# Performance work log

Measured on AMD Instinct MI355X. Metric: run time of the kernel, lower is better.

The kernel has to match this reference:

```python
import jax, jax.numpy as jnp
import numpy as np
import math

B, L, CS, CZ = 1, 512, 256, 128
H, CH, PQ, PV = 8, 32, 4, 8
NUM_BLOCKS = 8
CAT = H * CH + H * PV * 3 + H * PV + H * CZ  # 1536


def _ln(x, g, b, eps=1e-5):
    mu = jnp.mean(x, -1, keepdims=True)
    var = jnp.mean((x - mu) ** 2, -1, keepdims=True)
    return (x - mu) * jax.lax.rsqrt(var + eps) * g + b


def _quat_to_rot(bq, cq, dq):
    # BackboneUpdate: quaternion with implicit a=1, normalized (AF2 Alg. 23)
    norm = jnp.sqrt(1.0 + bq * bq + cq * cq + dq * dq)
    a = 1.0 / norm
    b = bq / norm
    c = cq / norm
    d = dq / norm
    return jnp.stack([
        jnp.stack([a * a + b * b - c * c - d * d, 2 * (b * c - a * d), 2 * (b * d + a * c)], -1),
        jnp.stack([2 * (b * c + a * d), a * a - b * b + c * c - d * d, 2 * (c * d - a * b)], -1),
        jnp.stack([2 * (b * d - a * c), 2 * (c * d + a * b), a * a - b * b - c * c + d * d], -1),
    ], -2)


def _forward(s, z, mask, ln_s_g, ln_s_b, ln_z_g, ln_z_b, w_init, b_init,
             ln_ipa_g, ln_ipa_b, ln_tr_g, ln_tr_b,
             wq, bq, wk, bk, wv, bv, wqp, bqp, wkp, bkp, wvp, bvp,
             wpb, head_w, wo, bo, wt1, bt1, wt2, bt2, wt3, bt3, wbb, bbb):
    s0 = _ln(s, ln_s_g, ln_s_b)
    zn = _ln(z, ln_z_g, ln_z_b)
    sc = s0 @ w_init + b_init
    R = jnp.broadcast_to(jnp.eye(3, dtype=s.dtype), (B, L, 3, 3))
    t = jnp.zeros((B, L, 3), s.dtype)
    wL = math.sqrt(1.0 / 3.0)
    wC = math.sqrt(2.0 / (9.0 * PQ))
    gamma = jax.nn.softplus(head_w)  # [H]
    pair_bias = jnp.einsum('bijc,ch->bhij', zn, wpb)
    mask_bias = (mask[:, None, None, :] - 1.0) * 1e9
    for i in range(NUM_BLOCKS):
        # ---- Invariant Point Attention (AF2 Alg. 22, shared weights) ----
        q = (sc @ wq + bq).reshape(B, L, H, CH)
        k = (sc @ wk + bk).reshape(B, L, H, CH)
        v = (sc @ wv + bv).reshape(B, L, H, CH)
        qp = (sc @ wqp + bqp).reshape(B, L, H, PQ, 3)
        kp = (sc @ wkp + bkp).reshape(B, L, H, PQ, 3)
        vp = (sc @ wvp + bvp).reshape(B, L, H, PV, 3)
        tb = t[:, :, None, None, :]
        qpg = jnp.einsum('blij,blhpj->blhpi', R, qp) + tb  # local -> global
        kpg = jnp.einsum('blij,blhpj->blhpi', R, kp) + tb
        vpg = jnp.einsum('blij,blhpj->blhpi', R, vp) + tb
        scal = jnp.einsum('bihc,bjhc->bhij', q, k) / math.sqrt(CH)
        # sum_p ||qpg_i - kpg_j||^2 via |q|^2 + |k|^2 - 2 q.k (avoids [B,L,L,H,P,3])
        qk = jnp.einsum('bihpx,bjhpx->bhij', qpg, kpg)
        qn = jnp.moveaxis(jnp.sum(qpg ** 2, axis=(-2, -1)), -1, 1)  # [B,H,L]
        kn = jnp.moveaxis(jnp.sum(kpg ** 2, axis=(-2, -1)), -1, 1)
        d2 = qn[..., :, None] + kn[..., None, :] - 2.0 * qk  # [B,H,L,L]
        logits = wL * (scal + pair_bias - 0.5 * wC * gamma[None, :, None, None] * d2) + mask_bias
        a = jax.nn.softmax(logits, axis=-1)
        o = jnp.einsum('bhij,bjhc->bihc', a, v).reshape(B, L, H * CH)
        optg = jnp.einsum('bhij,bjhpx->bihpx', a, vpg)
        optl = jnp.einsum('blji,blhpj->blhpi', R, optg - tb)  # R^T (o - t)
        onrm = jnp.sqrt(jnp.sum(optl ** 2, -1) + 1e-8)  # [B,L,H,PV]
        opair = jnp.einsum('bhij,bijc->bihc', a, zn).reshape(B, L, H * CZ)
        cat = jnp.concatenate([o, optl.reshape(B, L, H * PV * 3), onrm.reshape(B, L, H * PV), opair], -1)
        ipa_up = cat @ wo + bo
        sc = _ln(sc + ipa_up, ln_ipa_g, ln_ipa_b)  # dropout = identity (eval)
        # ---- transition ----
        tr = jax.nn.relu(sc @ wt1 + bt1)
        tr = jax.nn.relu(tr @ wt2 + bt2)
        tr = (tr @ wt3 + bt3) * mask[..., None]
        sc = _ln(sc + tr, ln_tr_g, ln_tr_b)
        # ---- backbone update + frame composition ----
        upd = sc @ wbb + bbb  # [B,L,6]
        dR = _quat_to_rot(upd[..., 0], upd[..., 1], upd[..., 2])
        dt = upd[..., 3:6] * mask[..., None]
        t = jnp.einsum('blij,blj->bli', R, dt) + t
        R = jnp.einsum('blij,bljk->blik', R, dR)
        if i < NUM_BLOCKS - 1:
            R = jax.lax.stop_gradient(R)  # stop_rotation_gradients
    return sc, R, t


def setup_inputs() -> dict:
    key = jax.random.key(0)
    ks = jax.random.split(key, 20)
    w = lambda k, shape, sc=0.05: jax.random.normal(k, shape, jnp.float32) * sc
    inp = dict(
        s=jax.random.normal(ks[0], (B, L, CS), jnp.float32),
        z=jax.random.normal(ks[1], (B, L, L, CZ), jnp.float32),
        mask=jnp.ones((B, L), jnp.float32),
        ln_s_g=jnp.ones((CS,), jnp.float32), ln_s_b=jnp.zeros((CS,), jnp.float32),
        ln_z_g=jnp.ones((CZ,), jnp.float32), ln_z_b=jnp.zeros((CZ,), jnp.float32),
        w_init=w(ks[2], (CS, CS)), b_init=jnp.zeros((CS,), jnp.float32),
        ln_ipa_g=jnp.ones((CS,), jnp.float32), ln_ipa_b=jnp.zeros((CS,), jnp.float32),
        ln_tr_g=jnp.ones((CS,), jnp.float32), ln_tr_b=jnp.zeros((CS,), jnp.float32),
        wq=w(ks[3], (CS, H * CH)), bq=jnp.zeros((H * CH,), jnp.float32),
        wk=w(ks[4], (CS, H * CH)), bk=jnp.zeros((H * CH,), jnp.float32),
        wv=w(ks[5], (CS, H * CH)), bv=jnp.zeros((H * CH,), jnp.float32),
        wqp=w(ks[6], (CS, H * PQ * 3)), bqp=jnp.zeros((H * PQ * 3,), jnp.float32),
        wkp=w(ks[7], (CS, H * PQ * 3)), bkp=jnp.zeros((H * PQ * 3,), jnp.float32),
        wvp=w(ks[8], (CS, H * PV * 3)), bvp=jnp.zeros((H * PV * 3,), jnp.float32),
        wpb=w(ks[9], (CZ, H)),
        head_w=jnp.zeros((H,), jnp.float32),
        wo=w(ks[10], (CAT, CS), 0.02), bo=jnp.zeros((CS,), jnp.float32),
        wt1=w(ks[11], (CS, CS)), bt1=jnp.zeros((CS,), jnp.float32),
        wt2=w(ks[12], (CS, CS)), bt2=jnp.zeros((CS,), jnp.float32),
        wt3=w(ks[13], (CS, CS)), bt3=jnp.zeros((CS,), jnp.float32),
        wbb=w(ks[14], (CS, 6)), bbb=jnp.zeros((6,), jnp.float32),
    )
    return inp


def reference(s, z, mask, ln_s_g, ln_s_b, ln_z_g, ln_z_b, w_init, b_init,
              ln_ipa_g, ln_ipa_b, ln_tr_g, ln_tr_b,
              wq, bq, wk, bk, wv, bv, wqp, bqp, wkp, bkp, wvp, bvp,
              wpb, head_w, wo, bo, wt1, bt1, wt2, bt2, wt3, bt3, wbb, bbb):
    return _forward(s, z, mask, ln_s_g, ln_s_b, ln_z_g, ln_z_b, w_init, b_init,
                    ln_ipa_g, ln_ipa_b, ln_tr_g, ln_tr_b,
                    wq, bq, wk, bk, wv, bv, wqp, bqp, wkp, bkp, wvp, bvp,
                    wpb, head_w, wo, bo, wt1, bt1, wt2, bt2, wt3, bt3, wbb, bbb)
```

## Files before the change

### kernel.cpp

```cpp
#include <hip/hip_runtime.h>
#include <hip/hip_bf16.h>
#include <hip/hip_fp16.h>
#include <math.h>

#define Lq 512
#define CSd 256
#define CZd 128
#define Hd 8
#define CHd 32
#define PQd 4
#define PVd 8
#define CATd 1536
#define NPROJ 1152

typedef __attribute__((ext_vector_type(4))) float floatx4;
typedef __attribute__((ext_vector_type(8))) short shortx8;

#define OFF_SC      0
#define OFF_PB      393216
#define OFF_P       1441792
#define OFF_QN      2031616
#define OFF_KN      2035712
#define OFF_A16     2039808
#define OFF_CAT     4136960
#define OFF_S0      4923392
#define OFF_R       5054464
#define OFF_T       5059072
#define OFF_GAMMA   5060608
#define OFF_MASKB   5060616
#define OFF_BCAT    5061128
#define OFF_WINITP  5062280
#define OFF_WT1P    5127816
#define OFF_WT2P    5193352
#define OFF_WT3P    5258888
#define OFF_WOP     5324424
#define OFF_WCATP   5717640
#define OFF_QP      6012552
#define OFF_KP      6274696
#define OFF_VP      6536840
#define OFF_ZNT     6798984

#define WLC 0.57735026918962576f
#define WCC 0.23570226039551584f
#define ISC 0.17677669529663687f

__device__ __forceinline__ float wave_sum(float v){
  #pragma unroll
  for (int m=32; m; m>>=1) v += __shfl_xor(v, m);
  return v;
}
__device__ __forceinline__ short f2bf(float v){
  __hip_bfloat16 h = (__hip_bfloat16)v;
  return __builtin_bit_cast(short, h);
}
__device__ __forceinline__ float bf2f(short s){
  unsigned u = ((unsigned)(unsigned short)s) << 16;
  return __builtin_bit_cast(float, u);
}
__device__ __forceinline__ __hip_bfloat16 s2b(short s){
  return __builtin_bit_cast(__hip_bfloat16, s);
}

__global__ __launch_bounds__(256) void k_setup(
    const float* __restrict__ bq, const float* __restrict__ bk, const float* __restrict__ bv,
    const float* __restrict__ bqp, const float* __restrict__ bkp, const float* __restrict__ bvp,
    const float* __restrict__ head_w, const float* __restrict__ mask,
    float* __restrict__ bcat, float* __restrict__ gamma,
    float* __restrict__ maskb, float* __restrict__ R, float* __restrict__ t){
  int k = blockIdx.x*256 + threadIdx.x;
  if (k < NPROJ){
    float v;
    if      (k < 256) v = bq[k];
    else if (k < 512) v = bk[k-256];
    else if (k < 768) v = bv[k-512];
    else if (k < 864) v = bqp[k-768];
    else if (k < 960) v = bkp[k-864];
    else              v = bvp[k-960];
    bcat[k] = v;
    return;
  }
  k -= NPROJ;
  if (k < Hd){ gamma[k] = log1pf(expf(head_w[k])); return; }
  k -= Hd;
  if (k < Lq){ maskb[k] = (mask[k] - 1.f)*1e9f; return; }
  k -= Lq;
  if (k < Lq){
    #pragma unroll
    for (int ii=0; ii<9; ii++) R[k*9+ii] = (ii==0||ii==4||ii==8) ? 1.f : 0.f;
    t[k*3] = 0.f; t[k*3+1] = 0.f; t[k*3+2] = 0.f;
  }
}

__global__ __launch_bounds__(256) void k_pack(
    const float* __restrict__ W, int K, int N, __hip_bfloat16* __restrict__ out){
  int idx = blockIdx.x*256 + threadIdx.x;
  if (idx >= K*N) return;
  int j = idx & 7, lane = (idx>>3) & 63, rest = idx >> 9;
  int nt = N >> 4;
  int tn = rest % nt, tk = rest / nt;
  int k = tk*32 + (lane>>4)*8 + j;
  int n = tn*16 + (lane&15);
  float v = W[(size_t)k*N + n];
  short h = f2bf(v);
  short l = f2bf(v - bf2f(h));
  size_t base = (size_t)rest*1024 + (idx & 511);
  out[base]       = s2b(h);
  out[base + 512] = s2b(l);
}

__global__ __launch_bounds__(256) void k_pack_cat(
    const float* __restrict__ wq, const float* __restrict__ wk, const float* __restrict__ wv,
    const float* __restrict__ wqp, const float* __restrict__ wkp, const float* __restrict__ wvp,
    __hip_bfloat16* __restrict__ out){
  int idx = blockIdx.x*256 + threadIdx.x;
  if (idx >= CSd*NPROJ) return;
  int j = idx & 7, lane = (idx>>3) & 63, rest = idx >> 9;
  const int nt = NPROJ >> 4;
  int tn = rest % nt, tk = rest / nt;
  int k = tk*32 + (lane>>4)*8 + j;
  int n = tn*16 + (lane&15);
  float v;
  if      (n < 256) v = wq[k*256 + n];
  else if (n < 512) v = wk[k*256 + n-256];
  else if (n < 768) v = wv[k*256 + n-512];
  else if (n < 864) v = wqp[k*96 + n-768];
  else if (n < 960) v = wkp[k*96 + n-864];
  else              v = wvp[k*192 + n-960];
  short h = f2bf(v);
  short l = f2bf(v - bf2f(h));
  size_t base = (size_t)rest*1024 + (idx & 511);
  out[base]       = s2b(h);
  out[base + 512] = s2b(l);
}

template<int NST>
__global__ __launch_bounds__(256) void k_gemm_mfma(
    const float* __restrict__ A, int K,
    const __hip_bfloat16* __restrict__ Bp, int N,
    const float* __restrict__ bias,
    float* __restrict__ Cf,
    int relu, const float* __restrict__ rowscale){
  int tid = threadIdx.x;
  int wave = tid>>6, lane = tid&63;
  int i0 = blockIdx.y*64 + wave*16;
  int n0 = blockIdx.x*(NST*16);
  int quad = lane>>4, l16 = lane&15;
  floatx4 acc[NST] = {};
  const int ntiles = N >> 4;
  const float* arow = A + (size_t)(i0 + l16)*K + quad*8;
  const __hip_bfloat16* bbase = Bp + ((size_t)(n0>>4))*1024 + (size_t)(lane&63)*8;
  for (int k0=0; k0<K; k0+=32){
    float4 v0 = *(const float4*)(arow + k0);
    float4 v1 = *(const float4*)(arow + k0 + 4);
    float av[8] = {v0.x,v0.y,v0.z,v0.w,v1.x,v1.y,v1.z,v1.w};
    shortx8 ahi, alo;
    #pragma unroll
    for (int j=0; j<8; j++){
      short h = f2bf(av[j]);
      ahi[j] = h;
      alo[j] = f2bf(av[j] - bf2f(h));
    }
    const __hip_bfloat16* bt = bbase + (size_t)(k0>>5)*ntiles*1024;
    #pragma unroll
    for (int s=0; s<NST; s++){
      shortx8 bhi = *(const shortx8*)(bt + s*1024);
      shortx8 blo = *(const shortx8*)(bt + s*1024 + 512);
      acc[s] = __builtin_amdgcn_mfma_f32_16x16x32_bf16(ahi, bhi, acc[s], 0, 0, 0);
      acc[s] = __builtin_amdgcn_mfma_f32_16x16x32_bf16(alo, bhi, acc[s], 0, 0, 0);
      acc[s] = __builtin_amdgcn_mfma_f32_16x16x32_bf16(ahi, blo, acc[s], 0, 0, 0);
    }
  }
  #pragma unroll
  for (int s=0; s<NST; s++){
    int n = n0 + s*16 + l16;
    float bs = bias ? bias[n] : 0.f;
    #pragma unroll
    for (int r=0; r<4; r++){
      int m = i0 + quad*4 + r;
      float v = acc[s][r] + bs;
      if (relu) v = fmaxf(v, 0.f);
      if (rowscale) v *= rowscale[m];
      Cf[(size_t)m*N + n] = v;
    }
  }
}

__global__ __launch_bounds__(256) void k_addln(
    const float* __restrict__ x, const float* __restrict__ y,
    const float* __restrict__ g, const float* __restrict__ b,
    float* __restrict__ out){
  __shared__ float red[4];
  int row = blockIdx.x, tid = threadIdx.x;
  float v = x[row*CSd + tid];
  if (y) v += y[row*CSd + tid];
  int wid = tid>>6, lane = tid&63;
  float s = wave_sum(v);
  if (lane==0) red[wid] = s;
  __syncthreads();
  float mu = (red[0]+red[1]+red[2]+red[3]) * (1.f/CSd);
  __syncthreads();
  float d = v - mu;
  float s2 = wave_sum(d*d);
  if (lane==0) red[wid] = s2;
  __syncthreads();
  float var = (red[0]+red[1]+red[2]+red[3]) * (1.f/CSd);
  float rs = rsqrtf(var + 1e-5f);
  out[row*CSd + tid] = d*rs*g[tid] + b[tid];
}

__global__ __launch_bounds__(1024, 4) void k_lnz_pb(
    const float* __restrict__ z, const float* __restrict__ g, const float* __restrict__ b,
    const float* __restrict__ wpb, __half* __restrict__ pb, __hip_bfloat16* __restrict__ znt){
  __shared__ float Zt[64*129];
  __shared__ float wpbht[8*132];
  __shared__ float gl[128], bl[128];
  __shared__ float muL[64], rsL[64];
  int tid = threadIdx.x;
  size_t row0 = (size_t)blockIdx.x*64;
  int ib = (int)(row0 >> 9), j0 = (int)(row0 & 511);
  {
    int c = tid>>3, h = tid&7;
    wpbht[h*132 + c] = wpb[tid];
  }
  if (tid < 128){ gl[tid] = g[tid]; bl[tid] = b[tid]; }
  {
    int w = tid>>6, lane = tid&63;
    #pragma unroll
    for (int it=0; it<4; it++){
      int row = it*16 + w;
      const float2 v = *(const float2*)(z + (row0+row)*(size_t)CZd + lane*2);
      Zt[row*129 + lane*2]     = v.x;
      Zt[row*129 + lane*2 + 1] = v.y;
    }
  }
  __syncthreads();
  {
    int r = tid>>4, q = tid&15;
    int rot = 2*(q>>2);
    float S1=0.f, S2=0.f;
    float zv[8];
    #pragma unroll
    for (int i=0; i<8; i++){
      int ii = (i + rot) & 7;
      float v = Zt[r*129 + q*8 + ii];
      zv[i] = v;
      S1 += v; S2 += v*v;
    }
    S1 += __shfl_xor(S1,1); S2 += __shfl_xor(S2,1);
    S1 += __shfl_xor(S1,2); S2 += __shfl_xor(S2,2);
    S1 += __shfl_xor(S1,4); S2 += __shfl_xor(S2,4);
    S1 += __shfl_xor(S1,8); S2 += __shfl_xor(S2,8);
    float mu = S1 * (1.f/128.f);
    float var = S2 * (1.f/128.f) - mu*mu;
    float rs = rsqrtf(var + 1e-5f);
    if (q == 0){ muL[r] = mu; rsL[r] = rs; }
    float d[8] = {};
    #pragma unroll
    for (int i=0; i<8; i++){
      int ii = (i + rot) & 7;
      int c = q*8 + ii;
      float znv = (zv[i]-mu)*rs*gl[c] + bl[c];
      #pragma unroll
      for (int h=0; h<8; h++) d[h] += znv * wpbht[h*132 + c];
    }
    #pragma unroll
    for (int h=0; h<8; h++){
      d[h] += __shfl_xor(d[h],1);
      d[h] += __shfl_xor(d[h],2);
      d[h] += __shfl_xor(d[h],4);
      d[h] += __shfl_xor(d[h],8);
    }
    if (q == 0){
      #pragma unroll
      for (int h=0; h<8; h++)
        pb[((size_t)(h*Lq + ib))*Lq + j0 + r] = __float2half(d[h]);
    }
  }
  __syncthreads();
  {
    int jj = (tid&31)*2, cidx = tid>>5;
    float mu0 = muL[jj],   rs0 = rsL[jj];
    float mu1 = muL[jj+1], rs1 = rsL[jj+1];
    unsigned short* zo = (unsigned short*)znt;
    #pragma unroll
    for (int it=0; it<4; it++){
      int c = it*32 + cidx;
      float gv = gl[c], bv = bl[c];
      float z0 = (Zt[jj*129 + c]     - mu0)*rs0*gv + bv;
      float z1 = (Zt[(jj+1)*129 + c] - mu1)*rs1*gv + bv;
      unsigned int o = ((unsigned int)(unsigned short)f2bf(z0)) |
                       (((unsigned int)(unsigned short)f2bf(z1)) << 16);
      *(unsigned int*)(zo + ((size_t)(ib*128 + c))*512 + j0 + jj) = o;
    }
  }
}

__global__ __launch_bounds__(256) void k_packqkv(
    const float* __restrict__ P, const float* __restrict__ R, const float* __restrict__ t,
    const float* __restrict__ gamma, int zfill,
    float* __restrict__ Qp, __hip_bfloat16* __restrict__ Kp, __hip_bfloat16* __restrict__ Vp,
    float* __restrict__ qn, float* __restrict__ kn){
  int idx = blockIdx.x*256 + threadIdx.x;
  int region = idx >> 15;
  int rem = idx & 32767;
  if (region == 0){
    int oct = rem & 7, h = (rem>>3)&7, j = rem>>6;
    float v[8] = {0.f,0.f,0.f,0.f,0.f,0.f,0.f,0.f};
    const float* Prow = P + (size_t)j*NPROJ;
    if (oct < 4){
      float4 a = *(const float4*)(Prow + 256 + h*CHd + oct*8);
      float4 b4 = *(const float4*)(Prow + 256 + h*CHd + oct*8 + 4);
      v[0]=a.x; v[1]=a.y; v[2]=a.z; v[3]=a.w; v[4]=b4.x; v[5]=b4.y; v[6]=b4.z; v[7]=b4.w;
    } else if (oct < 6){
      const float* kp = Prow + 864 + h*12;
      float4 k0 = *(const float4*)kp;
      float4 k1 = *(const float4*)(kp+4);
      float4 k2 = *(const float4*)(kp+8);
      float kv[12] = {k0.x,k0.y,k0.z,k0.w,k1.x,k1.y,k1.z,k1.w,k2.x,k2.y,k2.z,k2.w};
      float Rl[9];
      #pragma unroll
      for (int ii=0; ii<9; ii++) Rl[ii] = R[j*9+ii];
      float tv[3] = {t[j*3], t[j*3+1], t[j*3+2]};
      float gvals[12];
      #pragma unroll
      for (int p=0; p<4; p++)
        #pragma unroll
        for (int ax=0; ax<3; ax++)
          gvals[p*3+ax] = Rl[ax*3]*kv[p*3] + Rl[ax*3+1]*kv[p*3+1] + Rl[ax*3+2]*kv[p*3+2] + tv[ax];
      if (oct == 4){
        #pragma unroll
        for (int m=0; m<8; m++) v[m] = gvals[m];
      } else {
        #pragma unroll
        for (int m=0; m<4; m++) v[m] = gvals[8+m];
        float acc = 0.f;
        #pragma unroll
        for (int m=0; m<12; m++) acc += gvals[m]*gvals[m];
        kn[j*Hd + h] = acc;
      }
    } else {
      if (!zfill) return;
    }
    shortx8 hi, lo;
    #pragma unroll
    for (int m=0; m<8; m++){
      short hh = f2bf(v[m]);
      hi[m] = hh; lo[m] = f2bf(v[m] - bf2f(hh));
    }
    int kc = oct>>2, jt = j>>4, l16 = j&15, quad = oct&3;
    size_t base = (size_t)((h*2+kc)*32 + jt)*1024 + (quad*16+l16)*8;
    short* kp16 = (short*)Kp;
    *(shortx8*)(kp16 + base)       = hi;
    *(shortx8*)(kp16 + base + 512) = lo;
  } else if (region == 1){
    int n = rem & 63, h = (rem>>6)&7, jg = rem>>9;
    int jb = jg*8;
    float v[8] = {0.f,0.f,0.f,0.f,0.f,0.f,0.f,0.f};
    if (n < 32){
      #pragma unroll
      for (int m=0; m<8; m++) v[m] = P[(size_t)(jb+m)*NPROJ + 512 + h*CHd + n];
    } else if (n < 56){
      int p = (n-32)/3, ax = (n-32)%3;
      #pragma unroll
      for (int m=0; m<8; m++){
        int j = jb+m;
        const float* vp = P + (size_t)j*NPROJ + 960 + h*24 + p*3;
        const float* Rr = R + j*9 + ax*3;
        v[m] = Rr[0]*vp[0] + Rr[1]*vp[1] + Rr[2]*vp[2] + t[j*3+ax];
      }
    } else {
      if (!zfill) return;
    }
    shortx8 hi, lo;
    #pragma unroll
    for (int m=0; m<8; m++){
      short hh = f2bf(v[m]);
      hi[m] = hh; lo[m] = f2bf(v[m] - bf2f(hh));
    }
    int kc2 = jg>>2, w = n>>4, l16 = n&15, quad = jg&3;
    size_t base = (size_t)((h*16+kc2)*4 + w)*1024 + (quad*16+l16)*8;
    short* vp16 = (short*)Vp;
    *(shortx8*)(vp16 + base)       = hi;
    *(shortx8*)(vp16 + base + 512) = lo;
  } else {
    int oct = rem & 7, h = (rem>>3)&7, i = rem>>6;
    float v[8] = {0.f,0.f,0.f,0.f,0.f,0.f,0.f,0.f};
    const float* Prow = P + (size_t)i*NPROJ;
    if (oct < 4){
      float4 a = *(const float4*)(Prow + h*CHd + oct*8);
      float4 b4 = *(const float4*)(Prow + h*CHd + oct*8 + 4);
      const float sc = WLC*ISC;
      v[0]=a.x*sc; v[1]=a.y*sc; v[2]=a.z*sc; v[3]=a.w*sc;
      v[4]=b4.x*sc; v[5]=b4.y*sc; v[6]=b4.z*sc; v[7]=b4.w*sc;
    } else if (oct < 6){
      const float* qp = Prow + 768 + h*12;
      float4 k0 = *(const float4*)qp;
      float4 k1 = *(const float4*)(qp+4);
      float4 k2 = *(const float4*)(qp+8);
      float kv[12] = {k0.x,k0.y,k0.z,k0.w,k1.x,k1.y,k1.z,k1.w,k2.x,k2.y,k2.z,k2.w};
      float Rl[9];
      #pragma unroll
      for (int ii=0; ii<9; ii++) Rl[ii] = R[i*9+ii];
      float tv[3] = {t[i*3], t[i*3+1], t[i*3+2]};
      float gvals[12];
      #pragma unroll
      for (int p=0; p<4; p++)
        #pragma unroll
        for (int ax=0; ax<3; ax++)
          gvals[p*3+ax] = Rl[ax*3]*kv[p*3] + Rl[ax*3+1]*kv[p*3+1] + Rl[ax*3+2]*kv[p*3+2] + tv[ax];
      float sc = WLC*WCC*gamma[h];
      if (oct == 4){
        #pragma unroll
        for (int m=0; m<8; m++) v[m] = gvals[m]*sc;
      } else {
        #pragma unroll
        for (int m=0; m<4; m++) v[m] = gvals[8+m]*sc;
        float acc = 0.f;
        #pragma unroll
        for (int m=0; m<12; m++) acc += gvals[m]*gvals[m];
        qn[i*Hd + h] = acc;
      }
    } else {
      if (!zfill) return;
    }
    float* qrow = Qp + ((size_t)h*512 + i)*64 + oct*8;
    *(float4*)qrow       = make_float4(v[0],v[1],v[2],v[3]);
    *(float4*)(qrow + 4) = make_float4(v[4],v[5],v[6],v[7]);
  }
}

__global__ __launch_bounds__(512) void k_attn(
    const float* __restrict__ Qp, const __hip_bfloat16* __restrict__ Kp,
    const __hip_bfloat16* __restrict__ Vp,
    const float* __restrict__ qn, const float* __restrict__ kn,
    const __half* __restrict__ pb, const float* __restrict__ maskb,
    const float* __restrict__ gamma,
    const float* __restrict__ R, const float* __restrict__ t,
    __hip_bfloat16* __restrict__ a16hi,
    float* __restrict__ cat){
  __shared__ float At[16][516];
  __shared__ short AbfH[16*4*16*8];
  __shared__ short AbfL[16*4*16*8];
  __shared__ float Ot[16][36];
  __shared__ float Pv[16][68];
  __shared__ float red1[16][32];
  __shared__ float red2[16][32];
  __shared__ float invL[16];
  __shared__ float qnL[16];
  int tid = threadIdx.x;
  int i0 = blockIdx.x*16, h = blockIdx.y;
  int wave = tid>>6, lane = tid&63, quad = lane>>4, l16 = lane&15;
  int half = wave>>2, w4 = wave&3;
  float gam = gamma[h];
  float coef = 0.5f*WLC*WCC*gam;
  if (tid < 16) qnL[tid] = qn[(i0+tid)*Hd + h];
  __syncthreads();
  const float* qrow = Qp + ((size_t)h*512 + i0 + l16)*64 + quad*8;
  shortx8 qhi[2], qlo[2];
  #pragma unroll
  for (int kc=0; kc<2; kc++){
    float4 v0 = *(const float4*)(qrow + kc*32);
    float4 v1 = *(const float4*)(qrow + kc*32 + 4);
    float av[8] = {v0.x,v0.y,v0.z,v0.w,v1.x,v1.y,v1.z,v1.w};
    #pragma unroll
    for (int j=0; j<8; j++){
      short hh = f2bf(av[j]);
      qhi[kc][j] = hh; qlo[kc][j] = f2bf(av[j] - bf2f(hh));
    }
  }
  #pragma unroll
  for (int it=0; it<4; it++){
    int jt = it*8 + wave;
    floatx4 acc = {};
    #pragma unroll
    for (int kc=0; kc<2; kc++){
      const __hip_bfloat16* bt = Kp + (size_t)((h*2+kc)*32 + jt)*1024 + lane*8;
      shortx8 bhi = *(const shortx8*)bt;
      shortx8 blo = *(const shortx8*)(bt + 512);
      acc = __builtin_amdgcn_mfma_f32_16x16x32_bf16(qhi[kc], bhi, acc, 0, 0, 0);
      acc = __builtin_amdgcn_mfma_f32_16x16x32_bf16(qlo[kc], bhi, acc, 0, 0, 0);
      acc = __builtin_amdgcn_mfma_f32_16x16x32_bf16(qhi[kc], blo, acc, 0, 0, 0);
    }
    int j = jt*16 + l16;
    float knj = kn[j*Hd + h];
    float mbj = maskb[j];
    #pragma unroll
    for (int r=0; r<4; r++){
      int i = quad*4 + r;
      float pbv = __half2float(pb[((size_t)(h*Lq) + i0 + i)*Lq + j]);
      At[i][j] = acc[r] + WLC*pbv + mbj - coef*(qnL[i] + knj);
    }
  }
  __syncthreads();
  int srow = tid>>5, sseg = tid&31;
  {
    float m = -1e30f;
    #pragma unroll 8
    for (int k2=0; k2<16; k2++) m = fmaxf(m, At[srow][sseg + k2*32]);
    red1[srow][sseg] = m;
  }
  __syncthreads();
  float mrow = red1[srow][0];
  #pragma unroll
  for (int c=1;c<32;c++) mrow = fmaxf(mrow, red1[srow][c]);
  {
    float ssum = 0.f;
    #pragma unroll 8
    for (int k2=0; k2<16; k2++){
      int cc = sseg + k2*32;
      float e = __expf(At[srow][cc]-mrow);
      At[srow][cc] = e; ssum += e;
    }
    red2[srow][sseg] = ssum;
  }
  __syncthreads();
  if (tid < 16){
    float s=0.f;
    #pragma unroll
    for (int c=0;c<32;c++) s += red2[tid][c];
    invL[tid] = 1.f/s;
  }
  __syncthreads();
  for (int idx2=tid; idx2<8192; idx2+=512){
    int rr = idx2>>9, cc = idx2&511;
    float v = At[rr][cc]*invL[rr];
    size_t ai = (((size_t)(i0+rr)*16 + (cc>>5))*8 + h)*32 + (cc&31);
    short hh = f2bf(v);
    a16hi[ai] = s2b(hh);
    int off = ((((cc>>5)*4 + ((cc>>3)&3))*16 + rr)<<3) + (cc&7);
    AbfH[off] = hh;
    AbfL[off] = f2bf(v - bf2f(hh));
  }
  __syncthreads();
  floatx4 acc2 = {};
  #pragma unroll
  for (int kk=0; kk<8; kk++){
    int kc2 = half*8 + kk;
    int aoff = (((kc2*4 + quad)*16 + l16))<<3;
    shortx8 ahi = *(const shortx8*)&AbfH[aoff];
    shortx8 alo = *(const shortx8*)&AbfL[aoff];
    const __hip_bfloat16* bt = Vp + (size_t)((h*16+kc2)*4 + w4)*1024 + lane*8;
    shortx8 bhi = *(const shortx8*)bt;
    shortx8 blo = *(const shortx8*)(bt + 512);
    acc2 = __builtin_amdgcn_mfma_f32_16x16x32_bf16(ahi, bhi, acc2, 0, 0, 0);
    acc2 = __builtin_amdgcn_mfma_f32_16x16x32_bf16(alo, bhi, acc2, 0, 0, 0);
    acc2 = __builtin_amdgcn_mfma_f32_16x16x32_bf16(ahi, blo, acc2, 0, 0, 0);
  }
  if (half == 1){
    #pragma unroll
    for (int r=0;r<4;r++) Pv[quad*4+r][w4*16+l16] = acc2[r];
  }
  __syncthreads();
  if (half == 0){
    int n = w4*16 + l16;
    #pragma unroll
    for (int r=0;r<4;r++){
      int i = quad*4+r;
      float v = acc2[r] + Pv[i][n];
      if (n < 32) cat[(size_t)(i0+i)*CATd + h*CHd + n] = v;
      else        Ot[i][n-32] = v;
    }
  }
  __syncthreads();
  if (tid < 128){
    int i = tid>>3, p = tid&7, gi = i0+i;
    float o0 = Ot[i][p*3], o1 = Ot[i][p*3+1], o2 = Ot[i][p*3+2];
    float d0 = o0 - t[gi*3], d1 = o1 - t[gi*3+1], d2 = o2 - t[gi*3+2];
    const float* Rm = R + gi*9;
    float l0 = Rm[0]*d0 + Rm[3]*d1 + Rm[6]*d2;
    float l1 = Rm[1]*d0 + Rm[4]*d1 + Rm[7]*d2;
    float l2 = Rm[2]*d0 + Rm[5]*d1 + Rm[8]*d2;
    float* cr = cat + (size_t)gi*CATd;
    cr[256 + h*24 + p*3]   = l0;
    cr[256 + h*24 + p*3+1] = l1;
    cr[256 + h*24 + p*3+2] = l2;
    cr[448 + h*8 + p] = sqrtf(l0*l0 + l1*l1 + l2*l2 + 1e-8f);
  }
}

__global__ __launch_bounds__(256) void k_opair_mfma(
    const __hip_bfloat16* __restrict__ a16hi,
    const __hip_bfloat16* __restrict__ znt, float* __restrict__ cat){
  int i = blockIdx.x;
  int tid = threadIdx.x;
  int wave = tid>>6, lane = tid&63, quad = lane>>4, l16 = lane&15;
  int nt0 = wave*2, nt1 = wave*2+1;
  floatx4 acc0 = {}, acc1 = {};
  const __hip_bfloat16* abase_h = a16hi + ((size_t)i*16*8 + (l16&7))*32 + quad*8;
  const __hip_bfloat16* zb0 = znt + ((size_t)i*128 + nt0*16 + l16)*512 + quad*8;
  const __hip_bfloat16* zb1 = znt + ((size_t)i*128 + nt1*16 + l16)*512 + quad*8;
  #pragma unroll
  for (int kt=0; kt<16; kt++){
    shortx8 ah = *(const shortx8*)(abase_h + kt*256);
    shortx8 b0 = *(const shortx8*)(zb0 + kt*32);
    shortx8 b1 = *(const shortx8*)(zb1 + kt*32);
    acc0 = __builtin_amdgcn_mfma_f32_16x16x32_bf16(ah, b0, acc0, 0, 0, 0);
    acc1 = __builtin_amdgcn_mfma_f32_16x16x32_bf16(ah, b1, acc1, 0, 0, 0);
  }
  if (quad < 2){
    float* cr = cat + (size_t)i*CATd + 512;
    #pragma unroll
    for (int r=0; r<4; r++){
      int h = quad*4 + r;
      cr[h*CZd + nt0*16 + l16] = acc0[r];
      cr[h*CZd + nt1*16 + l16] = acc1[r];
    }
  }
}

__device__ __forceinline__ void gemm_bf8(
    const short* __restrict__ AHp, const short* __restrict__ ALp,
    short* __restrict__ OH, short* __restrict__ OL, float (*Yf)[260],
    const __hip_bfloat16* __restrict__ Wp, const float* __restrict__ bias,
    bool relu, int tid){
  int wave = tid>>6, lane = tid&63, quad = lane>>4, l16 = lane&15;
  floatx4 acc[2] = {};
  for (int kc=0; kc<8; kc++){
    int aoff = (((kc*4 + quad)*16 + l16))<<3;
    shortx8 ahi = *(const shortx8*)&AHp[aoff];
    shortx8 alo = *(const shortx8*)&ALp[aoff];
    #pragma unroll
    for (int ns=0; ns<2; ns++){
      const __hip_bfloat16* bt = Wp + (size_t)(kc*16 + wave*2 + ns)*1024 + lane*8;
      shortx8 bhi = *(const shortx8*)bt;
      shortx8 blo = *(const shortx8*)(bt + 512);
      acc[ns] = __builtin_amdgcn_mfma_f32_16x16x32_bf16(ahi, bhi, acc[ns], 0, 0, 0);
      acc[ns] = __builtin_amdgcn_mfma_f32_16x16x32_bf16(alo, bhi, acc[ns], 0, 0, 0);
      acc[ns] = __builtin_amdgcn_mfma_f32_16x16x32_bf16(ahi, blo, acc[ns], 0, 0, 0);
    }
  }
  #pragma unroll
  for (int ns=0; ns<2; ns++){
    int n = (wave*2+ns)*16 + l16;
    float bs = bias[n];
    #pragma unroll
    for (int r=0;r<4;r++){
      float v = acc[ns][r] + bs;
      if (relu) v = fmaxf(v, 0.f);
      int row = quad*4 + r;
      if (OH){
        short hh = f2bf(v);
        int off = ((((n>>5)*4 + ((n>>3)&3))*16 + row)<<3) + (n&7);
        OH[off] = hh;
        OL[off] = f2bf(v - bf2f(hh));
      } else {
        Yf[row][n] = v;
      }
    }
  }
}

__global__ __launch_bounds__(512) void k_mega(
    float* __restrict__ scb, const float* __restrict__ ipa,
    const float* __restrict__ gi_, const float* __restrict__ bi_,
    const __hip_bfloat16* __restrict__ W1, const float* __restrict__ c1,
    const __hip_bfloat16* __restrict__ W2, const float* __restrict__ c2,
    const __hip_bfloat16* __restrict__ W3, const float* __restrict__ c3,
    const float* __restrict__ gt_, const float* __restrict__ bt_,
    const float* __restrict__ mask,
    const float* __restrict__ wbb, const float* __restrict__ bbb,
    float* __restrict__ R, float* __restrict__ t){
  __shared__ float As[16][260], Bs[16][260];
  __shared__ short AH[2][4096], AL[2][4096];
  __shared__ float rA[16][33], rB[16][33];
  __shared__ float mv[16][2];
  __shared__ float u6p[16][6][2];
  int tid = threadIdx.x;
  int i0 = blockIdx.x*16;
  int r = tid>>5, c5 = tid&31, c0 = c5*8;
  float v[8];
  {
    const float* sr = scb + (size_t)(i0+r)*CSd + c0;
    const float* ir = ipa + (size_t)(i0+r)*CSd + c0;
    float s1=0.f, s2=0.f;
    #pragma unroll
    for (int k2=0;k2<8;k2++){ float x = sr[k2] + ir[k2]; v[k2]=x; s1+=x; s2+=x*x; }
    rA[r][c5]=s1; rB[r][c5]=s2;
  }
  __syncthreads();
  if (tid<16){
    float s1=0.f,s2=0.f;
    #pragma unroll
    for (int c=0;c<32;c++){ s1+=rA[tid][c]; s2+=rB[tid][c]; }
    float mu = s1*(1.f/CSd), var = s2*(1.f/CSd) - mu*mu;
    mv[tid][0]=mu; mv[tid][1]=rsqrtf(var+1e-5f);
  }
  __syncthreads();
  {
    float mu=mv[r][0], rs=mv[r][1];
    #pragma unroll
    for (int k2=0;k2<8;k2++){
      int col = c0+k2;
      float o = (v[k2]-mu)*rs*gi_[col] + bi_[col];
      As[r][col] = o;
      short hh = f2bf(o);
      int off = ((((col>>5)*4 + ((col>>3)&3))*16 + r)<<3) + (col&7);
      AH[0][off] = hh;
      AL[0][off] = f2bf(o - bf2f(hh));
    }
  }
  __syncthreads();
  gemm_bf8(AH[0], AL[0], AH[1], AL[1], nullptr, W1, c1, true, tid);
  __syncthreads();
  gemm_bf8(AH[1], AL[1], AH[0], AL[0], nullptr, W2, c2, true, tid);
  __syncthreads();
  gemm_bf8(AH[0], AL[0], nullptr, nullptr, Bs, W3, c3, false, tid);
  __syncthreads();
  {
    float mk = mask[i0+r];
    float s1=0.f, s2=0.f;
    #pragma unroll
    for (int k2=0;k2<8;k2++){ float x = As[r][c0+k2] + Bs[r][c0+k2]*mk; v[k2]=x; s1+=x; s2+=x*x; }
    rA[r][c5]=s1; rB[r][c5]=s2;
  }
  __syncthreads();
  if (tid<16){
    float s1=0.f,s2=0.f;
    #pragma unroll
    for (int c=0;c<32;c++){ s1+=rA[tid][c]; s2+=rB[tid][c]; }
    float mu = s1*(1.f/CSd), var = s2*(1.f/CSd) - mu*mu;
    mv[tid][0]=mu; mv[tid][1]=rsqrtf(var+1e-5f);
  }
  __syncthreads();
  {
    float mu=mv[r][0], rs=mv[r][1];
    float* out = scb + (size_t)(i0+r)*CSd + c0;
    #pragma unroll
    for (int k2=0;k2<8;k2++){
      int col = c0+k2;
      float o = (v[k2]-mu)*rs*gt_[col] + bt_[col];
      As[r][col] = o;
      out[k2] = o;
    }
  }
  __syncthreads();
  if (tid < 192){
    int rr = tid/12, o = (tid%12)>>1, half = tid&1;
    float acc = half ? 0.f : bbb[o];
    int kb = half*128;
    for (int k2=kb; k2<kb+128; k2++) acc += As[rr][k2]*wbb[k2*6+o];
    u6p[rr][o][half] = acc;
  }
  __syncthreads();
  if (tid < 16){
    int gidx = i0 + tid;
    float uu[6];
    #pragma unroll
    for (int o=0;o<6;o++) uu[o] = u6p[tid][o][0] + u6p[tid][o][1];
    float bq = uu[0], cq = uu[1], dq = uu[2];
    float norm = sqrtf(1.f + bq*bq + cq*cq + dq*dq);
    float a = 1.f/norm, b_ = bq/norm, c_ = cq/norm, d_ = dq/norm;
    float dR[9];
    dR[0] = a*a + b_*b_ - c_*c_ - d_*d_; dR[1] = 2.f*(b_*c_ - a*d_); dR[2] = 2.f*(b_*d_ + a*c_);
    dR[3] = 2.f*(b_*c_ + a*d_); dR[4] = a*a - b_*b_ + c_*c_ - d_*d_; dR[5] = 2.f*(c_*d_ - a*b_);
    dR[6] = 2.f*(b_*d_ - a*c_); dR[7] = 2.f*(c_*d_ + a*b_); dR[8] = a*a - b_*b_ - c_*c_ + d_*d_;
    float mk = mask[gidx];
    float dt0 = uu[3]*mk, dt1 = uu[4]*mk, dt2 = uu[5]*mk;
    float Rm[9];
    #pragma unroll
    for (int ii=0; ii<9; ii++) Rm[ii] = R[gidx*9+ii];
    t[gidx*3]   += Rm[0]*dt0 + Rm[1]*dt1 + Rm[2]*dt2;
    t[gidx*3+1] += Rm[3]*dt0 + Rm[4]*dt1 + Rm[5]*dt2;
    t[gidx*3+2] += Rm[6]*dt0 + Rm[7]*dt1 + Rm[8]*dt2;
    #pragma unroll
    for (int ii=0; ii<3; ii++)
      #pragma unroll
      for (int jj=0; jj<3; jj++)
        R[gidx*9 + ii*3 + jj] = Rm[ii*3]*dR[jj] + Rm[ii*3+1]*dR[3+jj] + Rm[ii*3+2]*dR[6+jj];
  }
}

__global__ __launch_bounds__(256) void k_writeout(
    const float* __restrict__ sc, const float* __restrict__ R, const float* __restrict__ t,
    float* __restrict__ out){
  int idx = blockIdx.x*256 + threadIdx.x;
  if      (idx < 131072) out[idx] = sc[idx];
  else if (idx < 135680) out[idx] = R[idx-131072];
  else if (idx < 137216) out[idx] = t[idx-135680];
}

extern "C" void kernel_launch(void* const* d_in, const int* in_sizes, int n_in,
                              void* d_out, int out_size, void* d_ws, size_t ws_size,
                              hipStream_t stream){
  const float* s      = (const float*)d_in[0];
  const float* z      = (const float*)d_in[1];
  const float* mask   = (const float*)d_in[2];
  const float* ln_s_g = (const float*)d_in[3];
  const float* ln_s_b = (const float*)d_in[4];
  const float* ln_z_g = (const float*)d_in[5];
  const float* ln_z_b = (const float*)d_in[6];
  const float* w_init = (const float*)d_in[7];
  const float* b_init = (const float*)d_in[8];
  const float* ln_ipa_g = (const float*)d_in[9];
  const float* ln_ipa_b = (const float*)d_in[10];
  const float* ln_tr_g  = (const float*)d_in[11];
  const float* ln_tr_b  = (const float*)d_in[12];
  const float* wq = (const float*)d_in[13]; const float* bq = (const float*)d_in[14];
  const float* wk = (const float*)d_in[15]; const float* bk = (const float*)d_in[16];
  const float* wv = (const float*)d_in[17]; const float* bv = (const float*)d_in[18];
  const float* wqp = (const float*)d_in[19]; const float* bqp = (const float*)d_in[20];
  const float* wkp = (const float*)d_in[21]; const float* bkp = (const float*)d_in[22];
  const float* wvp = (const float*)d_in[23]; const float* bvp = (const float*)d_in[24];
  const float* wpb = (const float*)d_in[25];
  const float* head_w = (const float*)d_in[26];
  const float* wo = (const float*)d_in[27]; const float* bo = (const float*)d_in[28];
  const float* wt1 = (const float*)d_in[29]; const float* bt1 = (const float*)d_in[30];
  const float* wt2 = (const float*)d_in[31]; const float* bt2 = (const float*)d_in[32];
  const float* wt3 = (const float*)d_in[33]; const float* bt3 = (const float*)d_in[34];
  const float* wbb = (const float*)d_in[35]; const float* bbb = (const float*)d_in[36];

  float* W = (float*)d_ws;
  float* scb   = W + OFF_SC;
  __half*  pbb  = (__half*)(W + OFF_PB);
  float* Pb    = W + OFF_P;
  float* qnb   = W + OFF_QN;
  float* knb   = W + OFF_KN;
  __hip_bfloat16* a16hi = (__hip_bfloat16*)(W + OFF_A16);
  float* catb  = W + OFF_CAT;
  float* s0b   = W + OFF_S0;
  float* Rb    = W + OFF_R;
  float* tb    = W + OFF_T;
  float* gammab= W + OFF_GAMMA;
  float* maskb = W + OFF_MASKB;
  float* bcat  = W + OFF_BCAT;
  __hip_bfloat16* WinitP = (__hip_bfloat16*)(W + OFF_WINITP);
  __hip_bfloat16* Wt1P   = (__hip_bfloat16*)(W + OFF_WT1P);
  __hip_bfloat16* Wt2P   = (__hip_bfloat16*)(W + OFF_WT2P);
  __hip_bfloat16* Wt3P   = (__hip_bfloat16*)(W + OFF_WT3P);
  __hip_bfloat16* WoP    = (__hip_bfloat16*)(W + OFF_WOP);
  __hip_bfloat16* WcatP  = (__hip_bfloat16*)(W + OFF_WCATP);
  float* Qp = W + OFF_QP;
  __hip_bfloat16* Kp = (__hip_bfloat16*)(W + OFF_KP);
  __hip_bfloat16* Vp = (__hip_bfloat16*)(W + OFF_VP);
  __hip_bfloat16* znt = (__hip_bfloat16*)(W + OFF_ZNT);

  k_setup<<<9, 256, 0, stream>>>(bq,bk,bv,bqp,bkp,bvp, head_w, mask, bcat, gammab, maskb, Rb, tb);
  k_pack_cat<<<CSd*NPROJ/256, 256, 0, stream>>>(wq,wk,wv,wqp,wkp,wvp, WcatP);
  k_pack<<<256,  256, 0, stream>>>(w_init, CSd, CSd, WinitP);
  k_pack<<<1536, 256, 0, stream>>>(wo, CATd, CSd, WoP);
  k_pack<<<256,  256, 0, stream>>>(wt1, CSd, CSd, Wt1P);
  k_pack<<<256,  256, 0, stream>>>(wt2, CSd, CSd, Wt2P);
  k_pack<<<256,  256, 0, stream>>>(wt3, CSd, CSd, Wt3P);

  k_addln<<<Lq, 256, 0, stream>>>(s, nullptr, ln_s_g, ln_s_b, s0b);
  k_gemm_mfma<4><<<dim3(4,8), 256, 0, stream>>>(s0b, CSd, WinitP, CSd, b_init, scb, 0, nullptr);
  k_lnz_pb<<<Lq*Lq/64, 1024, 0, stream>>>(z, ln_z_g, ln_z_b, wpb, pbb, znt);

  for (int it=0; it<8; ++it){
    k_gemm_mfma<2><<<dim3(36,8), 256, 0, stream>>>(scb, CSd, WcatP, NPROJ, bcat, Pb, 0, nullptr);
    k_packqkv<<<384, 256, 0, stream>>>(Pb, Rb, tb, gammab, (it==0)?1:0,
                                       Qp, Kp, Vp, qnb, knb);
    k_attn<<<dim3(32,8), 512, 0, stream>>>(Qp, Kp, Vp, qnb, knb, pbb, maskb, gammab, Rb, tb,
                                           a16hi, catb);
    k_opair_mfma<<<Lq, 256, 0, stream>>>(a16hi, znt, catb);
    k_gemm_mfma<1><<<dim3(16,8), 256, 0, stream>>>(catb, CATd, WoP, CSd, bo, Pb, 0, nullptr);
    k_mega<<<32, 512, 0, stream>>>(scb, Pb, ln_ipa_g, ln_ipa_b,
                                   Wt1P, bt1, Wt2P, bt2, Wt3P, bt3,
                                   ln_tr_g, ln_tr_b, mask, wbb, bbb, Rb, tb);
  }
  k_writeout<<<536, 256, 0, stream>>>(scb, Rb, tb, (float*)d_out);
}
```

Baseline: 951.9 us.

## Split-K output projection, halve attention row tile, widen opair blocks, simplify LN-z

Adds a split-K GEMM for the output projection, writing two partial results that the mega kernel sums, so twice as many blocks run. The attention kernel now processes 8 query rows per block instead of 16, doubling the grid. Its softmax becomes one wave per row using shuffle reductions in place of shared-memory reductions. The pair-output kernel uses 512 threads with one N tile per wave, and the z layernorm kernel keeps normalized values in shared memory instead of recomputing them. In exchange, attention wastes half of each MFMA tile and the new split-K path adds an extra partial buffer read.

Measured after the change: 887.6 us. -6.8%, faster.

```diff
diff --git a/kernel.cpp b/kernel.cpp
--- a/kernel.cpp
+++ b/kernel.cpp
@@ -185,6 +185,44 @@
   }
 }
 
+__global__ __launch_bounds__(256) void k_gemm_ipa(
+    const float* __restrict__ A, const __hip_bfloat16* __restrict__ Bp,
+    const float* __restrict__ bias, float* __restrict__ C0, float* __restrict__ C1){
+  int tid = threadIdx.x;
+  int wave = tid>>6, lane = tid&63;
+  int ks = blockIdx.y >> 3;
+  int i0 = (blockIdx.y & 7)*64 + wave*16;
+  int n0 = blockIdx.x*16;
+  int quad = lane>>4, l16 = lane&15;
+  floatx4 acc = {};
+  const float* arow = A + (size_t)(i0 + l16)*CATd + ks*768 + quad*8;
+  const __hip_bfloat16* bbase = Bp + ((size_t)(ks*24*16 + (n0>>4)))*1024 + (size_t)lane*8;
+  for (int k0=0; k0<768; k0+=32){
+    float4 v0 = *(const float4*)(arow + k0);
+    float4 v1 = *(const float4*)(arow + k0 + 4);
+    float av[8] = {v0.x,v0.y,v0.z,v0.w,v1.x,v1.y,v1.z,v1.w};
+    shortx8 ahi, alo;
+    #pragma unroll
+    for (int j=0; j<8; j++){
+      short h = f2bf(av[j]);
+      ahi[j] = h;
+      alo[j] = f2bf(av[j] - bf2f(h));
+    }
+    const __hip_bfloat16* bt = bbase + (size_t)(k0>>5)*16*1024;
+    shortx8 bhi = *(const shortx8*)bt;
+    shortx8 blo = *(const shortx8*)(bt + 512);
+    acc = __builtin_amdgcn_mfma_f32_16x16x32_bf16(ahi, bhi, acc, 0, 0, 0);
+    acc = __builtin_amdgcn_mfma_f32_16x16x32_bf16(alo, bhi, acc, 0, 0, 0);
+    acc = __builtin_amdgcn_mfma_f32_16x16x32_bf16(ahi, blo, acc, 0, 0, 0);
+  }
+  float* C = ks ? C1 : C0;
+  int n = n0 + l16;
+  float bs = ks ? 0.f : bias[n];
+  #pragma unroll
+  for (int r=0; r<4; r++)
+    C[(size_t)(i0 + quad*4 + r)*CSd + n] = acc[r] + bs;
+}
+
 __global__ __launch_bounds__(256) void k_addln(
     const float* __restrict__ x, const float* __restrict__ y,
     const float* __restrict__ g, const float* __restrict__ b,
@@ -212,15 +250,14 @@
     const float* __restrict__ z, const float* __restrict__ g, const float* __restrict__ b,
     const float* __restrict__ wpb, __half* __restrict__ pb, __hip_bfloat16* __restrict__ znt){
   __shared__ float Zt[64*129];
-  __shared__ float wpbht[8*132];
+  __shared__ float wpbl[128*12];
   __shared__ float gl[128], bl[128];
-  __shared__ float muL[64], rsL[64];
   int tid = threadIdx.x;
   size_t row0 = (size_t)blockIdx.x*64;
   int ib = (int)(row0 >> 9), j0 = (int)(row0 & 511);
   {
     int c = tid>>3, h = tid&7;
-    wpbht[h*132 + c] = wpb[tid];
+    wpbl[c*12 + h] = wpb[tid];
   }
   if (tid < 128){ gl[tid] = g[tid]; bl[tid] = b[tid]; }
   {
@@ -253,15 +290,17 @@
     float mu = S1 * (1.f/128.f);
     float var = S2 * (1.f/128.f) - mu*mu;
     float rs = rsqrtf(var + 1e-5f);
-    if (q == 0){ muL[r] = mu; rsL[r] = rs; }
     float d[8] = {};
     #pragma unroll
     for (int i=0; i<8; i++){
       int ii = (i + rot) & 7;
       int c = q*8 + ii;
       float znv = (zv[i]-mu)*rs*gl[c] + bl[c];
-      #pragma unroll
-      for (int h=0; h<8; h++) d[h] += znv * wpbht[h*132 + c];
+      Zt[r*129 + c] = znv;
+      const float4 w0 = *(const float4*)&wpbl[c*12];
+      const float4 w1 = *(const float4*)&wpbl[c*12 + 4];
+      d[0] += znv*w0.x; d[1] += znv*w0.y; d[2] += znv*w0.z; d[3] += znv*w0.w;
+      d[4] += znv*w1.x; d[5] += znv*w1.y; d[6] += znv*w1.z; d[7] += znv*w1.w;
     }
     #pragma unroll
     for (int h=0; h<8; h++){
@@ -279,15 +318,12 @@
   __syncthreads();
   {
     int jj = (tid&31)*2, cidx = tid>>5;
-    float mu0 = muL[jj],   rs0 = rsL[jj];
-    float mu1 = muL[jj+1], rs1 = rsL[jj+1];
     unsigned short* zo = (unsigned short*)znt;
     #pragma unroll
     for (int it=0; it<4; it++){
       int c = it*32 + cidx;
-      float gv = gl[c], bv = bl[c];
-      float z0 = (Zt[jj*129 + c]     - mu0)*rs0*gv + bv;
-      float z1 = (Zt[(jj+1)*129 + c] - mu1)*rs1*gv + bv;
+      float z0 = Zt[jj*129 + c];
+      float z1 = Zt[(jj+1)*129 + c];
       unsigned int o = ((unsigned int)(unsigned short)f2bf(z0)) |
                        (((unsigned int)(unsigned short)f2bf(z1)) << 16);
       *(unsigned int*)(zo + ((size_t)(ib*128 + c))*512 + j0 + jj) = o;
@@ -438,24 +474,21 @@
     const float* __restrict__ R, const float* __restrict__ t,
     __hip_bfloat16* __restrict__ a16hi,
     float* __restrict__ cat){
-  __shared__ float At[16][516];
+  __shared__ float At[8][516];
   __shared__ short AbfH[16*4*16*8];
   __shared__ short AbfL[16*4*16*8];
-  __shared__ float Ot[16][36];
-  __shared__ float Pv[16][68];
-  __shared__ float red1[16][32];
-  __shared__ float red2[16][32];
-  __shared__ float invL[16];
-  __shared__ float qnL[16];
+  __shared__ float Ot[8][36];
+  __shared__ float Pv[8][68];
+  __shared__ float qnL[8];
   int tid = threadIdx.x;
-  int i0 = blockIdx.x*16, h = blockIdx.y;
+  int i0 = blockIdx.x*8, h = blockIdx.y;
   int wave = tid>>6, lane = tid&63, quad = lane>>4, l16 = lane&15;
   int half = wave>>2, w4 = wave&3;
   float gam = gamma[h];
   float coef = 0.5f*WLC*WCC*gam;
-  if (tid < 16) qnL[tid] = qn[(i0+tid)*Hd + h];
-  __syncthreads();
-  const float* qrow = Qp + ((size_t)h*512 + i0 + l16)*64 + quad*8;
+  if (tid < 8) qnL[tid] = qn[(i0+tid)*Hd + h];
+  __syncthreads();
+  const float* qrow = Qp + ((size_t)h*512 + i0 + (l16&7))*64 + quad*8;
   shortx8 qhi[2], qlo[2];
   #pragma unroll
   for (int kc=0; kc<2; kc++){
@@ -481,55 +514,46 @@
       acc = __builtin_amdgcn_mfma_f32_16x16x32_bf16(qlo[kc], bhi, acc, 0, 0, 0);
       acc = __builtin_amdgcn_mfma_f32_16x16x32_bf16(qhi[kc], blo, acc, 0, 0, 0);
     }
-    int j = jt*16 + l16;
-    float knj = kn[j*Hd + h];
-    float mbj = maskb[j];
-    #pragma unroll
-    for (int r=0; r<4; r++){
-      int i = quad*4 + r;
-      float pbv = __half2float(pb[((size_t)(h*Lq) + i0 + i)*Lq + j]);
-      At[i][j] = acc[r] + WLC*pbv + mbj - coef*(qnL[i] + knj);
-    }
-  }
-  __syncthreads();
-  int srow = tid>>5, sseg = tid&31;
+    if (quad < 2){
+      int j = jt*16 + l16;
+      float knj = kn[j*Hd + h];
+      float mbj = maskb[j];
+      #pragma unroll
+      for (int r=0; r<4; r++){
+        int i = quad*4 + r;
+        float pbv = __half2float(pb[((size_t)(h*Lq) + i0 + i)*Lq + j]);
+        At[i][j] = acc[r] + WLC*pbv + mbj - coef*(qnL[i] + knj);
+      }
+    }
+  }
+  __syncthreads();
   {
+    int w = wave;
+    float v[8];
     float m = -1e30f;
-    #pragma unroll 8
-    for (int k2=0; k2<16; k2++) m = fmaxf(m, At[srow][sseg + k2*32]);
-    red1[srow][sseg] = m;
-  }
-  __syncthreads();
-  float mrow = red1[srow][0];
-  #pragma unroll
-  for (int c=1;c<32;c++) mrow = fmaxf(mrow, red1[srow][c]);
-  {
+    #pragma unroll
+    for (int k=0; k<8; k++){ v[k] = At[w][lane + 64*k]; m = fmaxf(m, v[k]); }
+    #pragma unroll
+    for (int msk=32; msk; msk>>=1) m = fmaxf(m, __shfl_xor(m, msk));
     float ssum = 0.f;
-    #pragma unroll 8
-    for (int k2=0; k2<16; k2++){
-      int cc = sseg + k2*32;
-      float e = __expf(At[srow][cc]-mrow);
-      At[srow][cc] = e; ssum += e;
-    }
-    red2[srow][sseg] = ssum;
-  }
-  __syncthreads();
-  if (tid < 16){
-    float s=0.f;
-    #pragma unroll
-    for (int c=0;c<32;c++) s += red2[tid][c];
-    invL[tid] = 1.f/s;
-  }
-  __syncthreads();
-  for (int idx2=tid; idx2<8192; idx2+=512){
-    int rr = idx2>>9, cc = idx2&511;
-    float v = At[rr][cc]*invL[rr];
-    size_t ai = (((size_t)(i0+rr)*16 + (cc>>5))*8 + h)*32 + (cc&31);
-    short hh = f2bf(v);
-    a16hi[ai] = s2b(hh);
-    int off = ((((cc>>5)*4 + ((cc>>3)&3))*16 + rr)<<3) + (cc&7);
-    AbfH[off] = hh;
-    AbfL[off] = f2bf(v - bf2f(hh));
+    #pragma unroll
+    for (int k=0; k<8; k++){ float e = __expf(v[k]-m); v[k]=e; ssum += e; }
+    #pragma unroll
+    for (int msk=32; msk; msk>>=1) ssum += __shfl_xor(ssum, msk);
+    float inv = 1.f/ssum;
+    #pragma unroll
+    for (int k=0; k<8; k++){
+      int cc = lane + 64*k;
+      float p = v[k]*inv;
+      short hh = f2bf(p);
+      short ll = f2bf(p - bf2f(hh));
+      a16hi[(((size_t)(i0+w)*16 + (cc>>5))*8 + h)*32 + (cc&31)] = s2b(hh);
+      int base = ((cc>>5)*4 + ((cc>>3)&3))*16;
+      int off0 = ((base + w)<<3) + (cc&7);
+      int off1 = ((base + w + 8)<<3) + (cc&7);
+      AbfH[off0] = hh; AbfH[off1] = hh;
+      AbfL[off0] = ll; AbfL[off1] = ll;
+    }
   }
   __syncthreads();
   floatx4 acc2 = {};
@@ -546,12 +570,12 @@
     acc2 = __builtin_amdgcn_mfma_f32_16x16x32_bf16(alo, bhi, acc2, 0, 0, 0);
     acc2 = __builtin_amdgcn_mfma_f32_16x16x32_bf16(ahi, blo, acc2, 0, 0, 0);
   }
-  if (half == 1){
+  if (half == 1 && quad < 2){
     #pragma unroll
     for (int r=0;r<4;r++) Pv[quad*4+r][w4*16+l16] = acc2[r];
   }
   __syncthreads();
-  if (half == 0){
+  if (half == 0 && quad < 2){
     int n = w4*16 + l16;
     #pragma unroll
     for (int r=0;r<4;r++){
@@ -562,7 +586,7 @@
     }
   }
   __syncthreads();
-  if (tid < 128){
+  if (tid < 64){
     int i = tid>>3, p = tid&7, gi = i0+i;
     float o0 = Ot[i][p*3], o1 = Ot[i][p*3+1], o2 = Ot[i][p*3+2];
     float d0 = o0 - t[gi*3], d1 = o1 - t[gi*3+1], d2 = o2 - t[gi*3+2];
@@ -578,32 +602,28 @@
   }
 }
 
-__global__ __launch_bounds__(256) void k_opair_mfma(
+__global__ __launch_bounds__(512) void k_opair_mfma(
     const __hip_bfloat16* __restrict__ a16hi,
     const __hip_bfloat16* __restrict__ znt, float* __restrict__ cat){
   int i = blockIdx.x;
   int tid = threadIdx.x;
   int wave = tid>>6, lane = tid&63, quad = lane>>4, l16 = lane&15;
-  int nt0 = wave*2, nt1 = wave*2+1;
-  floatx4 acc0 = {}, acc1 = {};
+  int nt = wave;
+  floatx4 acc = {};
   const __hip_bfloat16* abase_h = a16hi + ((size_t)i*16*8 + (l16&7))*32 + quad*8;
-  const __hip_bfloat16* zb0 = znt + ((size_t)i*128 + nt0*16 + l16)*512 + quad*8;
-  const __hip_bfloat16* zb1 = znt + ((size_t)i*128 + nt1*16 + l16)*512 + quad*8;
+  const __hip_bfloat16* zb = znt + ((size_t)i*128 + nt*16 + l16)*512 + quad*8;
   #pragma unroll
   for (int kt=0; kt<16; kt++){
     shortx8 ah = *(const shortx8*)(abase_h + kt*256);
-    shortx8 b0 = *(const shortx8*)(zb0 + kt*32);
-    shortx8 b1 = *(const shortx8*)(zb1 + kt*32);
-    acc0 = __builtin_amdgcn_mfma_f32_16x16x32_bf16(ah, b0, acc0, 0, 0, 0);
-    acc1 = __builtin_amdgcn_mfma_f32_16x16x32_bf16(ah, b1, acc1, 0, 0, 0);
+    shortx8 b0 = *(const shortx8*)(zb + kt*32);
+    acc = __builtin_amdgcn_mfma_f32_16x16x32_bf16(ah, b0, acc, 0, 0, 0);
   }
   if (quad < 2){
     float* cr = cat + (size_t)i*CATd + 512;
     #pragma unroll
     for (int r=0; r<4; r++){
       int h = quad*4 + r;
-      cr[h*CZd + nt0*16 + l16] = acc0[r];
-      cr[h*CZd + nt1*16 + l16] = acc1[r];
+      cr[h*CZd + nt*16 + l16] = acc[r];
     }
   }
 }
@@ -651,7 +671,7 @@
 }
 
 __global__ __launch_bounds__(512) void k_mega(
-    float* __restrict__ scb, const float* __restrict__ ipa,
+    float* __restrict__ scb, const float* __restrict__ ipa, const float* __restrict__ ipa2,
     const float* __restrict__ gi_, const float* __restrict__ bi_,
     const __hip_bfloat16* __restrict__ W1, const float* __restrict__ c1,
     const __hip_bfloat16* __restrict__ W2, const float* __restrict__ c2,
@@ -672,9 +692,10 @@
   {
     const float* sr = scb + (size_t)(i0+r)*CSd + c0;
     const float* ir = ipa + (size_t)(i0+r)*CSd + c0;
+    const float* ir2 = ipa2 + (size_t)(i0+r)*CSd + c0;
     float s1=0.f, s2=0.f;
     #pragma unroll
-    for (int k2=0;k2<8;k2++){ float x = sr[k2] + ir[k2]; v[k2]=x; s1+=x; s2+=x*x; }
+    for (int k2=0;k2<8;k2++){ float x = sr[k2] + ir[k2] + ir2[k2]; v[k2]=x; s1+=x; s2+=x*x; }
     rA[r][c5]=s1; rB[r][c5]=s2;
   }
   __syncthreads();
@@ -813,6 +834,7 @@
   float* scb   = W + OFF_SC;
   __half*  pbb  = (__half*)(W + OFF_PB);
   float* Pb    = W + OFF_P;
+  float* ipa2b = W + OFF_P + 262144;
   float* qnb   = W + OFF_QN;
   float* knb   = W + OFF_KN;
   __hip_bfloat16* a16hi = (__hip_bfloat16*)(W + OFF_A16);
@@ -850,11 +872,11 @@
     k_gemm_mfma<2><<<dim3(36,8), 256, 0, stream>>>(scb, CSd, WcatP, NPROJ, bcat, Pb, 0, nullptr);
     k_packqkv<<<384, 256, 0, stream>>>(Pb, Rb, tb, gammab, (it==0)?1:0,
                                        Qp, Kp, Vp, qnb, knb);
-    k_attn<<<dim3(32,8), 512, 0, stream>>>(Qp, Kp, Vp, qnb, knb, pbb, maskb, gammab, Rb, tb,
+    k_attn<<<dim3(64,8), 512, 0, stream>>>(Qp, Kp, Vp, qnb, knb, pbb, maskb, gammab, Rb, tb,
                                            a16hi, catb);
-    k_opair_mfma<<<Lq, 256, 0, stream>>>(a16hi, znt, catb);
-    k_gemm_mfma<1><<<dim3(16,8), 256, 0, stream>>>(catb, CATd, WoP, CSd, bo, Pb, 0, nullptr);
-    k_mega<<<32, 512, 0, stream>>>(scb, Pb, ln_ipa_g, ln_ipa_b,
+    k_opair_mfma<<<Lq, 512, 0, stream>>>(a16hi, znt, catb);
+    k_gemm_ipa<<<dim3(16,16), 256, 0, stream>>>(catb, WoP, bo, Pb, ipa2b);
+    k_mega<<<32, 512, 0, stream>>>(scb, Pb, ipa2b, ln_ipa_g, ln_ipa_b,
                                    Wt1P, bt1, Wt2P, bt2, Wt3P, bt3,
                                    ln_tr_g, ln_tr_b, mask, wbb, bbb, Rb, tb);
   }
```
